# Performance work log

Measured on AMD Instinct MI355X. Metric: run time of the kernel, lower is better.

The kernel has to match this reference:

```python
import jax, jax.numpy as jnp
import numpy as np

N = 200000   # total nodes across batch
E = 800000   # total edges (avg degree 4)
G = 64       # number of graphs in batch
NGT = 30     # num gate types
EMB = 64     # gate_type_embed_dim
H = 128      # h_feats
INTER = 128  # inter_dim
EPS = 1e-12  # F.normalize eps


def _xavier(key, shape):
    fan_in, fan_out = shape
    std = np.sqrt(2.0 / (fan_in + fan_out))
    return jax.random.normal(key, shape, dtype=jnp.float32) * std


def setup_inputs() -> dict:
    key = jax.random.key(0)
    ks = jax.random.split(key, 12)
    gate_type = jax.random.randint(ks[0], (N,), 0, NGT)
    src = jax.random.randint(ks[1], (E,), 0, N)
    dst = jax.random.randint(ks[2], (E,), 0, N)
    w = jax.random.uniform(ks[3], (E, 3), dtype=jnp.float32)
    node2graph = (jnp.arange(N) * G) // N  # sorted segment ids, even split
    emb = jax.random.normal(ks[4], (NGT, EMB), dtype=jnp.float32)
    return {
        "gate_type": gate_type, "src": src, "dst": dst, "w": w,
        "node2graph": node2graph, "emb": emb,
        "W1_0": _xavier(ks[5], (EMB + 3, INTER)), "b1_0": jnp.zeros((INTER,), jnp.float32),
        "W2_0": _xavier(ks[6], (EMB + INTER, H)),
        "W1_1": _xavier(ks[7], (H + 3, INTER)), "b1_1": jnp.zeros((INTER,), jnp.float32),
        "W2_1": _xavier(ks[8], (H + INTER, H)),
        "W1_2": _xavier(ks[9], (H + 3, INTER)), "b1_2": jnp.zeros((INTER,), jnp.float32),
        "W2_2": _xavier(ks[10], (H + INTER, H)),
    }


def _qconv(h, src, dst, w, W1, b1, W2):
    # message: cat(h[src], w) per edge; linear1+ReLU per message; sum per dst node
    m = jnp.concatenate([h[src], w], axis=1)          # [E, in+3]
    t = jax.nn.relu(m @ W1 + b1)                      # [E, inter]
    h_N = jax.ops.segment_sum(t, dst, num_segments=h.shape[0])  # [N, inter]
    h_lin = jax.nn.relu(jnp.concatenate([h, h_N], axis=1) @ W2)  # [N, out]
    norm = jnp.linalg.norm(h_lin, axis=-1, keepdims=True)
    return h_lin / jnp.maximum(norm, EPS)             # F.normalize(p=2, dim=-1)


def reference(gate_type, src, dst, w, node2graph, emb,
              W1_0, b1_0, W2_0, W1_1, b1_1, W2_1, W1_2, b1_2, W2_2):
    h = emb[gate_type]                                # [N, EMB]
    layers = [(W1_0, b1_0, W2_0), (W1_1, b1_1, W2_1), (W1_2, b1_2, W2_2)]
    readouts = []
    for W1, b1, W2 in layers:
        h = _qconv(h, src, dst, w, W1, b1, W2)
        readouts.append(jax.ops.segment_sum(h, node2graph, num_segments=G))  # [G, H]
    return h, jnp.concatenate(readouts, axis=1)       # [N,H], [G, 3H]
```

## Files before the change

kernel.cpp:

```cpp
#include <hip/hip_runtime.h>
#include <hip/hip_bf16.h>
#include <hip/hip_fp16.h>

typedef _Float16 half8 __attribute__((ext_vector_type(8)));
typedef _Float16 half4 __attribute__((ext_vector_type(4)));
typedef _Float16 h2    __attribute__((ext_vector_type(2)));
typedef float floatx4 __attribute__((ext_vector_type(4)));

__device__ __forceinline__ _Float16 f2h(float f) { return (_Float16)f; }


__global__ void fill_dummy_kernel(int4* __restrict__ eData, int cap, int N, int NGT)
{
    int i = blockIdx.x * 256 + threadIdx.x;
    if (i < cap) { int4 v = {N | (NGT << 24), N, 0, 0}; eData[i] = v; }
}

__global__ void hist_kernel(const int* __restrict__ dst, int* __restrict__ cnt, int E)
{
    int e = blockIdx.x * 256 + threadIdx.x;
    if (e < E) atomicAdd(&cnt[dst[e]], 1);
}

__global__ void scan1p_kernel(const int* __restrict__ cnt, int* __restrict__ offP,
                              int n, int* __restrict__ blockSums)
{
    __shared__ int sm[256];
    const int t = threadIdx.x;
    const int base = blockIdx.x * 1024 + t * 4;
    int v[4]; int s = 0;
#pragma unroll
    for (int i = 0; i < 4; ++i) {
        v[i] = (base + i < n) ? ((cnt[base + i] + 3) & ~3) : 0;
        s += v[i];
    }
    sm[t] = s; __syncthreads();
#pragma unroll
    for (int off = 1; off < 256; off <<= 1) {
        int y = (t >= off) ? sm[t - off] : 0;
        __syncthreads();
        if (t >= off) sm[t] += y;
        __syncthreads();
    }
    int excl = sm[t] - s;
    if (t == 255) blockSums[blockIdx.x] = sm[255];
    int run = excl;
#pragma unroll
    for (int i = 0; i < 4; ++i) {
        if (base + i < n) offP[base + i] = run;
        run += v[i];
    }
}

__global__ void scan2_kernel(int* __restrict__ blockSums, int nb)
{
    __shared__ int sm[256];
    const int t = threadIdx.x;
    int s = (t < nb) ? blockSums[t] : 0;
    sm[t] = s; __syncthreads();
#pragma unroll
    for (int off = 1; off < 256; off <<= 1) {
        int y = (t >= off) ? sm[t - off] : 0;
        __syncthreads();
        if (t >= off) sm[t] += y;
        __syncthreads();
    }
    if (t < nb) blockSums[t] = sm[t] - s;
}

__global__ void scan3_kernel(int* __restrict__ offP, int n, const int* __restrict__ blockSums)
{
    const int base = blockIdx.x * 1024 + threadIdx.x * 4;
    const int add = blockSums[blockIdx.x];
#pragma unroll
    for (int i = 0; i < 4; ++i)
        if (base + i < n) offP[base + i] += add;
}

__global__ void scatter_kernel(const int* __restrict__ src, const int* __restrict__ dst,
                               const float* __restrict__ w, const int* __restrict__ gt,
                               const int* __restrict__ offP, int* __restrict__ cur,
                               int4* __restrict__ eData, int E)
{
    int e = blockIdx.x * 256 + threadIdx.x;
    if (e >= E) return;
    int d = dst[e];
    int p = offP[d] + atomicAdd(&cur[d], 1);
    int s = src[e];
    h2 w01 = { f2h(w[(size_t)e * 3 + 0]), f2h(w[(size_t)e * 3 + 1]) };
    h2 w2o = { f2h(w[(size_t)e * 3 + 2]), (_Float16)1.0f };
    int4 v = { s | (gt[s] << 24), d,
               __builtin_bit_cast(int, w01), __builtin_bit_cast(int, w2o) };
    eData[p] = v;
}

__global__ void ginfo_kernel(const int4* __restrict__ eData,
                             const int* __restrict__ cnt, const int* __restrict__ offP,
                             unsigned* __restrict__ gInfo,
                             int nGroups, int N, int gpw)
{
    int g = blockIdx.x * 256 + threadIdx.x;
    if (g >= nGroups) return;
    const int* ei = (const int*)eData;
    int d = ei[16 * g + 1];
    if (d >= N) { gInfo[g] = 0xFFFFFFFFu; return; }
    int cntP = (cnt[d] + 3) & ~3;
    int gA = offP[d] >> 2;
    int gB = gA + (cntP >> 2) - 1;
    bool cross = (gA / gpw) != (gB / gpw);
    gInfo[g] = (unsigned)d | (cross ? 0x80000000u : 0u);
}

__global__ void wprep_kernel(const float* __restrict__ W, _Float16* __restrict__ out,
                             int K, int KP)
{
    int idx = blockIdx.x * 256 + threadIdx.x;
    if (idx >= 128 * KP) return;
    int f = idx / KP, k = idx % KP;
    float v = (k < K) ? W[(size_t)k * 128 + f] : 0.0f;
    out[idx] = f2h(v);
}

__global__ void wwprep_kernel(const float* __restrict__ W1, int rowOff,
                              _Float16* __restrict__ out)
{
    int idx = blockIdx.x * 256 + threadIdx.x;
    if (idx < 3 * 128) out[idx] = f2h(W1[(size_t)(rowOff + idx / 128) * 128 + (idx & 127)]);
}

__global__ void embW1_kernel(const float* __restrict__ emb, const float* __restrict__ W1,
                             const float* __restrict__ b1, _Float16* __restrict__ out, int NGT)
{
    int idx = blockIdx.x * 256 + threadIdx.x;
    if (idx >= (NGT + 1) * 128) return;
    int g = idx >> 7, f = idx & 127;
    float s = 0.0f;
    if (g < NGT) {
        s = b1[f];
        for (int k = 0; k < 64; ++k) s += emb[g * 64 + k] * W1[(size_t)k * 128 + f];
    }
    out[idx] = f2h(s);
}

__global__ void embW2_kernel(const float* __restrict__ emb, const float* __restrict__ W2,
                             float* __restrict__ out, int NGT)
{
    int idx = blockIdx.x * 256 + threadIdx.x;
    if (idx >= NGT * 128) return;
    int g = idx >> 7, f = idx & 127;
    float s = 0.0f;
    for (int k = 0; k < 64; ++k) s += emb[g * 64 + k] * W2[(size_t)k * 128 + f];
    out[idx] = s;
}

__global__ void __launch_bounds__(512, 2)
hw1_kernel(const _Float16* __restrict__ hA,
           const _Float16* __restrict__ WT,
           const float* __restrict__ b1,
           _Float16* __restrict__ out,
           int N, int tilesPerWave, int nTiles)
{
    __shared__ __align__(16) _Float16 lds[128 * 128];
    const int tid = threadIdx.x;
    for (int s = tid; s < 128 * 16; s += 512) {
        const int row = s / 16, seg = s % 16;
        half8 v = *(const half8*)(WT + (size_t)row * 128 + seg * 8);
        *(half8*)(&lds[row * 128 + ((seg ^ (row & 7)) * 8)]) = v;
    }
    __syncthreads();

    const int lane = tid & 63;
    const int wv   = tid >> 6;
    const int lRow = lane & 15;
    const int lGrp = lane >> 4;

    float b1v[8];
#pragma unroll
    for (int jt = 0; jt < 8; ++jt) b1v[jt] = b1[jt * 16 + lRow];

    const int wave = blockIdx.x * 8 + wv;
    const int t0 = wave * tilesPerWave;
    const int t1 = min(t0 + tilesPerWave, nTiles);

    for (int tile = t0; tile < t1; ++tile) {
        const int i0 = tile * 16;
        const int iA = min(i0 + lRow, N - 1);
        half8 a[4];
#pragma unroll
        for (int kc = 0; kc < 4; ++kc)
            a[kc] = *(const half8*)(hA + (size_t)iA * 128 + kc * 32 + lGrp * 8);

        floatx4 acc[8] = {};
#pragma unroll
        for (int jt = 0; jt < 8; ++jt) {
            const int row = jt * 16 + lRow;
            const int sw = row & 7;
#pragma unroll
            for (int kc = 0; kc < 4; ++kc) {
                half8 b = *(const half8*)(&lds[row * 128 + (((kc * 4 + lGrp) ^ sw) * 8)]);
                acc[jt] = __builtin_amdgcn_mfma_f32_16x16x32_f16(a[kc], b, acc[jt], 0, 0, 0);
            }
        }
#pragma unroll
        for (int r = 0; r < 4; ++r) {
            const int i = i0 + lGrp * 4 + r;
            if (i < N) {
#pragma unroll
                for (int jt = 0; jt < 8; ++jt)
                    out[(size_t)i * 128 + jt * 16 + lRow] = f2h(acc[jt][r] + b1v[jt]);
            }
        }
    }
}

template<bool L0, bool H16>
__global__ void __launch_bounds__(256, 4)
edgeW_kernel(const _Float16* __restrict__ T,
             const _Float16* __restrict__ Wwh,
             const int4* __restrict__ eData,
             const unsigned* __restrict__ gInfo,
             void* __restrict__ hNv, int groupsPerWave, int nGroups)
{
    const int tid  = threadIdx.x;
    const int lane = tid & 63;
    const int wv   = tid >> 6;
    const int eidx = lane >> 4;
    const int c8   = (lane & 15) * 8;

    const h2 z = {(_Float16)0.0f, (_Float16)0.0f};
    h2 w0[4], w1[4], w2[4];
#pragma unroll
    for (int j = 0; j < 4; ++j) {
        w0[j] = *(const h2*)(Wwh + 0 * 128 + c8 + 2 * j);
        w1[j] = *(const h2*)(Wwh + 1 * 128 + c8 + 2 * j);
        w2[j] = *(const h2*)(Wwh + 2 * 128 + c8 + 2 * j);
    }

    const int wave = blockIdx.x * 4 + wv;
    const int g0 = wave * groupsPerWave;
    const int g1 = min(g0 + groupsPerWave, nGroups);
    if (g0 >= g1) return;

    int runD = -1; bool runCross = false;
    h2 a0 = z, a1 = z, a2 = z, a3 = z;

    auto flush = [&]() {
        if (runD < 0) return;
        h2 s0 = a0, s1 = a1, s2 = a2, s3 = a3;
#pragma unroll
        for (int m = 16; m <= 32; m <<= 1) {
            int t0_ = __shfl_xor(__builtin_bit_cast(int, s0), m);
            int t1_ = __shfl_xor(__builtin_bit_cast(int, s1), m);
            int t2_ = __shfl_xor(__builtin_bit_cast(int, s2), m);
            int t3_ = __shfl_xor(__builtin_bit_cast(int, s3), m);
            s0 = s0 + __builtin_bit_cast(h2, t0_);
            s1 = s1 + __builtin_bit_cast(h2, t1_);
            s2 = s2 + __builtin_bit_cast(h2, t2_);
            s3 = s3 + __builtin_bit_cast(h2, t3_);
        }
        if (lane < 16) {
            if (H16) {
                if (runCross) {
                    __half2* p = (__half2*)((__half*)hNv + (size_t)runD * 128 + c8);
                    unsafeAtomicAdd(p + 0, __builtin_bit_cast(__half2, s0));
                    unsafeAtomicAdd(p + 1, __builtin_bit_cast(__half2, s1));
                    unsafeAtomicAdd(p + 2, __builtin_bit_cast(__half2, s2));
                    unsafeAtomicAdd(p + 3, __builtin_bit_cast(__half2, s3));
                } else {
                    int4 pk = { __builtin_bit_cast(int, s0), __builtin_bit_cast(int, s1),
                                __builtin_bit_cast(int, s2), __builtin_bit_cast(int, s3) };
                    *(int4*)((__half*)hNv + (size_t)runD * 128 + c8) = pk;
                }
            } else {
                float f[8] = {(float)s0[0], (float)s0[1], (float)s1[0], (float)s1[1],
                              (float)s2[0], (float)s2[1], (float)s3[0], (float)s3[1]};
                float* p = (float*)hNv + (size_t)runD * 128 + c8;
                if (runCross) {
#pragma unroll
                    for (int j = 0; j < 8; ++j) unsafeAtomicAdd(p + j, f[j]);
                } else {
                    floatx4 q0 = {f[0], f[1], f[2], f[3]};
                    floatx4 q1 = {f[4], f[5], f[6], f[7]};
                    *(floatx4*)(p) = q0;
                    *(floatx4*)(p + 4) = q1;
                }
            }
        }
    };

    for (int g = g0; g < g1; ++g) {
        const unsigned gi = gInfo[g];
        if (gi == 0xFFFFFFFFu) break;
        const int dG = (int)(gi & 0xFFFFFFu);

        const int4 e = eData[g * 4 + eidx];
        const int r_ = L0 ? (e.x >> 24) : (e.x & 0xFFFFFF);
        const half8 Tv = *(const half8*)(T + (size_t)r_ * 128 + c8);
        const h2 w01 = __builtin_bit_cast(h2, e.z);
        const h2 w2o = __builtin_bit_cast(h2, e.w);

        h2 m0 = h2{Tv[0], Tv[1]} + w01[0] * w0[0] + w01[1] * w1[0] + w2o[0] * w2[0];
        h2 m1 = h2{Tv[2], Tv[3]} + w01[0] * w0[1] + w01[1] * w1[1] + w2o[0] * w2[1];
        h2 m2 = h2{Tv[4], Tv[5]} + w01[0] * w0[2] + w01[1] * w1[2] + w2o[0] * w2[2];
        h2 m3 = h2{Tv[6], Tv[7]} + w01[0] * w0[3] + w01[1] * w1[3] + w2o[0] * w2[3];
        h2 r0 = __builtin_elementwise_max(m0, z);
        h2 r1 = __builtin_elementwise_max(m1, z);
        h2 r2 = __builtin_elementwise_max(m2, z);
        h2 r3 = __builtin_elementwise_max(m3, z);

        if (dG == runD) {
            a0 = a0 + r0; a1 = a1 + r1; a2 = a2 + r2; a3 = a3 + r3;
        } else {
            flush();
            runD = dG; runCross = (gi >> 31) != 0;
            a0 = r0; a1 = r1; a2 = r2; a3 = r3;
        }
    }
    flush();
}

template<bool H16, bool L0, bool LAST>
__global__ void __launch_bounds__(512, 2)
node_kernel(const _Float16* __restrict__ hA,
            const void* __restrict__ hNv,
            const _Float16* __restrict__ W2T,
            const float* __restrict__ embW2,
            const int* __restrict__ gt,
            const int* __restrict__ n2g,
            _Float16* __restrict__ hOut,
            float* __restrict__ fOut,
            float* __restrict__ readout,
            int N, int tilesPerWave, int nTiles, int layerOff)
{
    constexpr int K2  = L0 ? 128 : 256;
    constexpr int KCA = L0 ? 0 : 4;
    constexpr int KC  = K2 / 32;
    constexpr int SPR = K2 / 8;
    __shared__ __align__(16) _Float16 lds[128 * K2];

    const int tid = threadIdx.x;
    for (int s = tid; s < 128 * SPR; s += 512) {
        const int row = s / SPR, seg = s % SPR;
        half8 v = *(const half8*)(W2T + (size_t)row * K2 + seg * 8);
        *(half8*)(&lds[row * K2 + ((seg ^ (row & 7)) * 8)]) = v;
    }
    __syncthreads();

    const int lane = tid & 63;
    const int wv   = tid >> 6;
    const int lRow = lane & 15;
    const int lGrp = lane >> 4;
    const int wave = blockIdx.x * 8 + wv;
    const int t0 = wave * tilesPerWave;
    const int t1 = min(t0 + tilesPerWave, nTiles);
    if (t0 >= t1) return;

    int gCur = -1; float racc[8];
#pragma unroll
    for (int jt = 0; jt < 8; ++jt) racc[jt] = 0.0f;

    auto loadA = [&](int i0, half8 (&afrag)[KC]) {
        const int iA = min(i0 + lRow, N - 1);
#pragma unroll
        for (int kc = 0; kc < KCA; ++kc)
            afrag[kc] = *(const half8*)(hA + (size_t)iA * 128 + kc * 32 + lGrp * 8);
        if (H16) {
            const _Float16* hN = (const _Float16*)hNv;
#pragma unroll
            for (int kc = KCA; kc < KC; ++kc)
                afrag[kc] = *(const half8*)(hN + (size_t)iA * 128 + (kc - KCA) * 32 + lGrp * 8);
        } else {
            const float* hN = (const float*)hNv;
#pragma unroll
            for (int kc = KCA; kc < KC; ++kc) {
                const float* p = hN + (size_t)iA * 128 + (kc - KCA) * 32 + lGrp * 8;
                floatx4 f0 = *(const floatx4*)(p);
                floatx4 f1 = *(const floatx4*)(p + 4);
                half8 a;
#pragma unroll
                for (int i = 0; i < 4; ++i) { a[i] = f2h(f0[i]); a[i + 4] = f2h(f1[i]); }
                afrag[kc] = a;
            }
        }
    };

    auto epilogue = [&](int i0, floatx4 (&acc)[8]) {
        if (L0) {
#pragma unroll
            for (int r = 0; r < 4; ++r) {
                const int i = min(i0 + lGrp * 4 + r, N - 1);
                const int g_t = gt[i];
#pragma unroll
                for (int jt = 0; jt < 8; ++jt)
                    acc[jt][r] += embW2[(size_t)g_t * 128 + jt * 16 + lRow];
            }
        }
        float scl[4];
#pragma unroll
        for (int r = 0; r < 4; ++r) {
            float s = 0.f;
#pragma unroll
            for (int jt = 0; jt < 8; ++jt) {
                float v = fmaxf(acc[jt][r], 0.0f);
                s += v * v;
            }
#pragma unroll
            for (int m = 1; m <= 8; m <<= 1) s += __shfl_xor(s, m);
            scl[r] = 1.0f / fmaxf(sqrtf(s), 1e-12f);
        }
#pragma unroll
        for (int r = 0; r < 4; ++r) {
            const int i = i0 + lGrp * 4 + r;
            if (i < N) {
#pragma unroll
                for (int jt = 0; jt < 8; ++jt) {
                    float v = fmaxf(acc[jt][r], 0.0f) * scl[r];
                    if (LAST) fOut[(size_t)i * 128 + jt * 16 + lRow] = v;
                    else      hOut[(size_t)i * 128 + jt * 16 + lRow] = f2h(v);
                }
            }
        }
        const int gFirst = n2g[min(i0, N - 1)];
        const int gLast  = n2g[min(i0 + 15, N - 1)];
        if (gFirst == gLast && i0 + 15 < N) {
            if (gFirst != gCur) {
                if (gCur >= 0 && lane < 16) {
#pragma unroll
                    for (int jt = 0; jt < 8; ++jt)
                        unsafeAtomicAdd(&readout[(size_t)gCur * 384 + layerOff + jt * 16 + lane], racc[jt]);
                }
                gCur = gFirst;
#pragma unroll
                for (int jt = 0; jt < 8; ++jt) racc[jt] = 0.0f;
            }
#pragma unroll
            for (int jt = 0; jt < 8; ++jt) {
                float t = 0.f;
#pragma unroll
                for (int r = 0; r < 4; ++r) t += fmaxf(acc[jt][r], 0.0f) * scl[r];
                t += __shfl_xor(t, 16);
                t += __shfl_xor(t, 32);
                racc[jt] += t;
            }
        } else {
            if (gCur >= 0 && lane < 16) {
#pragma unroll
                for (int jt = 0; jt < 8; ++jt)
                    unsafeAtomicAdd(&readout[(size_t)gCur * 384 + layerOff + jt * 16 + lane], racc[jt]);
            }
            gCur = -1;
#pragma unroll
            for (int jt = 0; jt < 8; ++jt) racc[jt] = 0.0f;
#pragma unroll
            for (int r = 0; r < 4; ++r) {
                const int i = i0 + lGrp * 4 + r;
                if (i < N) {
                    const int g = n2g[i];
#pragma unroll
                    for (int jt = 0; jt < 8; ++jt) {
                        float v = fmaxf(acc[jt][r], 0.0f) * scl[r];
                        unsafeAtomicAdd(&readout[(size_t)g * 384 + layerOff + jt * 16 + lRow], v);
                    }
                }
            }
        }
    };

    for (int tile = t0; tile < t1; tile += 2) {
        const bool has2 = (tile + 1 < t1);
        const int i0a = tile * 16;
        const int i0b = has2 ? (tile + 1) * 16 : i0a;

        half8 afA[KC], afB[KC];
        loadA(i0a, afA);
        loadA(i0b, afB);

        floatx4 accA[8] = {}, accB[8] = {};
#pragma unroll
        for (int jt = 0; jt < 8; ++jt) {
            const int rb = (jt * 16 + lRow) * K2;
            const int sw = (jt * 16 + lRow) & 7;
#pragma unroll
            for (int kc = 0; kc < KC; ++kc) {
                half8 b = *(const half8*)(&lds[rb + (((kc * 4 + lGrp) ^ sw) * 8)]);
                accA[jt] = __builtin_amdgcn_mfma_f32_16x16x32_f16(afA[kc], b, accA[jt], 0, 0, 0);
                accB[jt] = __builtin_amdgcn_mfma_f32_16x16x32_f16(afB[kc], b, accB[jt], 0, 0, 0);
            }
        }
        epilogue(i0a, accA);
        if (has2) epilogue(i0b, accB);
    }
    if (gCur >= 0 && lane < 16) {
#pragma unroll
        for (int jt = 0; jt < 8; ++jt)
            unsafeAtomicAdd(&readout[(size_t)gCur * 384 + layerOff + jt * 16 + lane], racc[jt]);
    }
}

extern "C" void kernel_launch(void* const* d_in, const int* in_sizes, int n_in,
                              void* d_out, int out_size, void* d_ws, size_t ws_size,
                              hipStream_t stream)
{
    const int*   gate_type = (const int*)d_in[0];
    const int*   src  = (const int*)d_in[1];
    const int*   dst  = (const int*)d_in[2];
    const float* wE   = (const float*)d_in[3];
    const int*   n2g  = (const int*)d_in[4];
    const float* emb  = (const float*)d_in[5];
    const float* W1_0 = (const float*)d_in[6];
    const float* b1_0 = (const float*)d_in[7];
    const float* W2_0 = (const float*)d_in[8];
    const float* W1_1 = (const float*)d_in[9];
    const float* b1_1 = (const float*)d_in[10];
    const float* W2_1 = (const float*)d_in[11];
    const float* W1_2 = (const float*)d_in[12];
    const float* b1_2 = (const float*)d_in[13];
    const float* W2_2 = (const float*)d_in[14];

    const int N = in_sizes[0];
    const int E = in_sizes[1];
    const int NGT = in_sizes[5] / 64;
    const int cap = (E + 3 * N + 15) & ~15;

    char* ws = (char*)d_ws;
    size_t off = 0;
    auto alloc = [&](size_t bytes) { void* p = ws + off; off = (off + bytes + 255) & ~255ULL; return p; };
    _Float16* hBuf  = (_Float16*)alloc((size_t)N * 128 * 2);
    int4*     eData = (int4*)alloc(((size_t)cap + 16) * 16);
    unsigned* gInfo = (unsigned*)alloc(((size_t)cap / 4 + 4) * 4);
    int*      cnt   = (int*)alloc((size_t)N * 4);
    int*      offP  = (int*)alloc((size_t)N * 4);
    int*      cur   = (int*)alloc((size_t)N * 4);
    int*      bSums = (int*)alloc(256 * 4);
    _Float16* W1T1  = (_Float16*)alloc((size_t)128 * 128 * 2);
    _Float16* W1T2  = (_Float16*)alloc((size_t)128 * 128 * 2);
    _Float16* W2T0  = (_Float16*)alloc((size_t)128 * 128 * 2);
    _Float16* W2T1  = (_Float16*)alloc((size_t)128 * 256 * 2);
    _Float16* W2T2  = (_Float16*)alloc((size_t)128 * 256 * 2);
    _Float16* Wwh0  = (_Float16*)alloc((size_t)3 * 128 * 2);
    _Float16* Wwh1  = (_Float16*)alloc((size_t)3 * 128 * 2);
    _Float16* Wwh2  = (_Float16*)alloc((size_t)3 * 128 * 2);
    _Float16* eW1b  = (_Float16*)alloc((size_t)(NGT + 1) * 128 * 2);
    float*    eW2   = (float*)alloc((size_t)NGT * 128 * 4);
    _Float16* hW1b  = (_Float16*)alloc(((size_t)N + 1) * 128 * 2);
    size_t hn16_off = off;
    const bool h16 = (ws_size >= hn16_off + (size_t)N * 128 * 2 + 256);
    _Float16* hN16 = (_Float16*)alloc((size_t)N * 128 * 2);

    float* readout = (float*)d_out + (size_t)N * 128;
    void*  hN      = h16 ? (void*)hN16 : (void*)d_out;

    const int nGroups = cap / 4;
    const int nTiles  = (N + 15) / 16;
    const int EB = 2048;
    const int gpw = (nGroups + EB * 4 - 1) / (EB * 4);
    const int NB = 256;
    const int tpwN = (nTiles + NB * 8 - 1) / (NB * 8);
    const int HB = 256;
    const int tpwH = (nTiles + HB * 8 - 1) / (HB * 8);
    const int nb = (N + 1023) / 1024;

    hipMemsetAsync(cnt, 0, (size_t)N * 4, stream);
    hipMemsetAsync(cur, 0, (size_t)N * 4, stream);
    hipMemsetAsync(hW1b + (size_t)N * 128, 0, 256, stream);
    fill_dummy_kernel<<<(cap + 16 + 255) / 256, 256, 0, stream>>>(eData, cap + 16, N, NGT);
    hist_kernel<<<(E + 255) / 256, 256, 0, stream>>>(dst, cnt, E);
    scan1p_kernel<<<nb, 256, 0, stream>>>(cnt, offP, N, bSums);
    scan2_kernel<<<1, 256, 0, stream>>>(bSums, nb);
    scan3_kernel<<<nb, 256, 0, stream>>>(offP, N, bSums);
    scatter_kernel<<<(E + 255) / 256, 256, 0, stream>>>(src, dst, wE, gate_type,
                                                        offP, cur, eData, E);
    ginfo_kernel<<<(nGroups + 255) / 256, 256, 0, stream>>>(eData, cnt, offP, gInfo,
                                                            nGroups, N, gpw);

    embW1_kernel<<<((NGT + 1) * 128 + 255) / 256, 256, 0, stream>>>(emb, W1_0, b1_0, eW1b, NGT);
    embW2_kernel<<<(NGT * 128 + 255) / 256, 256, 0, stream>>>(emb, W2_0, eW2, NGT);
    wprep_kernel<<<(128 * 128 + 255) / 256, 256, 0, stream>>>(W1_1, W1T1, 128, 128);
    wprep_kernel<<<(128 * 128 + 255) / 256, 256, 0, stream>>>(W1_2, W1T2, 128, 128);
    wprep_kernel<<<(128 * 128 + 255) / 256, 256, 0, stream>>>(W2_0 + (size_t)64 * 128, W2T0, 128, 128);
    wprep_kernel<<<(128 * 256 + 255) / 256, 256, 0, stream>>>(W2_1, W2T1, 256, 256);
    wprep_kernel<<<(128 * 256 + 255) / 256, 256, 0, stream>>>(W2_2, W2T2, 256, 256);
    wwprep_kernel<<<2, 256, 0, stream>>>(W1_0, 64, Wwh0);
    wwprep_kernel<<<2, 256, 0, stream>>>(W1_1, 128, Wwh1);
    wwprep_kernel<<<2, 256, 0, stream>>>(W1_2, 128, Wwh2);

    if (h16) {
        hipMemsetAsync(readout, 0, (size_t)(out_size - N * 128) * 4, stream);
        hipMemsetAsync(hN16, 0, (size_t)N * 128 * 2, stream);
        edgeW_kernel<true, true><<<EB, 256, 0, stream>>>(eW1b, Wwh0, eData, gInfo, hN, gpw, nGroups);
        node_kernel<true, true, false><<<NB, 512, 0, stream>>>(nullptr, hN, W2T0, eW2, gate_type, n2g,
                                                               hBuf, nullptr, readout, N, tpwN, nTiles, 0);
        hw1_kernel<<<HB, 512, 0, stream>>>(hBuf, W1T1, b1_1, hW1b, N, tpwH, nTiles);
        hipMemsetAsync(hN16, 0, (size_t)N * 128 * 2, stream);
        edgeW_kernel<false, true><<<EB, 256, 0, stream>>>(hW1b, Wwh1, eData, gInfo, hN, gpw, nGroups);
        node_kernel<true, false, false><<<NB, 512, 0, stream>>>(hBuf, hN, W2T1, nullptr, nullptr, n2g,
                                                                hBuf, nullptr, readout, N, tpwN, nTiles, 128);
        hw1_kernel<<<HB, 512, 0, stream>>>(hBuf, W1T2, b1_2, hW1b, N, tpwH, nTiles);
        hipMemsetAsync(hN16, 0, (size_t)N * 128 * 2, stream);
        edgeW_kernel<false, true><<<EB, 256, 0, stream>>>(hW1b, Wwh2, eData, gInfo, hN, gpw, nGroups);
        node_kernel<true, false, true><<<NB, 512, 0, stream>>>(hBuf, hN, W2T2, nullptr, nullptr, n2g,
                                                               nullptr, (float*)d_out, readout, N, tpwN, nTiles, 256);
    } else {
        hipMemsetAsync(d_out, 0, (size_t)out_size * 4, stream);
        edgeW_kernel<true, false><<<EB, 256, 0, stream>>>(eW1b, Wwh0, eData, gInfo, hN, gpw, nGroups);
        node_kernel<false, true, false><<<NB, 512, 0, stream>>>(nullptr, hN, W2T0, eW2, gate_type, n2g,
                                                                hBuf, nullptr, readout, N, tpwN, nTiles, 0);
        hw1_kernel<<<HB, 512, 0, stream>>>(hBuf, W1T1, b1_1, hW1b, N, tpwH, nTiles);
        hipMemsetAsync(d_out, 0, (size_t)N * 128 * 4, stream);
        edgeW_kernel<false, false><<<EB, 256, 0, stream>>>(hW1b, Wwh1, eData, gInfo, hN, gpw, nGroups);
        node_kernel<false, false, false><<<NB, 512, 0, stream>>>(hBuf, hN, W2T1, nullptr, nullptr, n2g,
                                                                 hBuf, nullptr, readout, N, tpwN, nTiles, 128);
        hw1_kernel<<<HB, 512, 0, stream>>>(hBuf, W1T2, b1_2, hW1b, N, tpwH, nTiles);
        hipMemsetAsync(d_out, 0, (size_t)N * 128 * 4, stream);
        edgeW_kernel<false, false><<<EB, 256, 0, stream>>>(hW1b, Wwh2, eData, gInfo, hN, gpw, nGroups);
        node_kernel<false, false, true><<<NB, 512, 0, stream>>>(hBuf, hN, W2T2, nullptr, nullptr, n2g,
                                                                nullptr, (float*)d_out, readout, N, tpwN, nTiles, 256);
    }
}
```

Baseline: 504.5 us.

## Zero only boundary and isolated hN rows; record edge ranks in histogram pass

```diff
diff --git a/kernel.cpp b/kernel.cpp
--- a/kernel.cpp
+++ b/kernel.cpp
@@ -16,10 +16,11 @@
     if (i < cap) { int4 v = {N | (NGT << 24), N, 0, 0}; eData[i] = v; }
 }
 
-__global__ void hist_kernel(const int* __restrict__ dst, int* __restrict__ cnt, int E)
+__global__ void histrank_kernel(const int* __restrict__ dst, int* __restrict__ cnt,
+                                int* __restrict__ rank, int E)
 {
     int e = blockIdx.x * 256 + threadIdx.x;
-    if (e < E) atomicAdd(&cnt[dst[e]], 1);
+    if (e < E) rank[e] = atomicAdd(&cnt[dst[e]], 1);
 }
 
 __global__ void scan1p_kernel(const int* __restrict__ cnt, int* __restrict__ offP,
@@ -79,13 +80,13 @@
 
 __global__ void scatter_kernel(const int* __restrict__ src, const int* __restrict__ dst,
                                const float* __restrict__ w, const int* __restrict__ gt,
-                               const int* __restrict__ offP, int* __restrict__ cur,
+                               const int* __restrict__ offP, const int* __restrict__ rank,
                                int4* __restrict__ eData, int E)
 {
     int e = blockIdx.x * 256 + threadIdx.x;
     if (e >= E) return;
     int d = dst[e];
-    int p = offP[d] + atomicAdd(&cur[d], 1);
+    int p = offP[d] + rank[e];
     int s = src[e];
     h2 w01 = { f2h(w[(size_t)e * 3 + 0]), f2h(w[(size_t)e * 3 + 1]) };
     h2 w2o = { f2h(w[(size_t)e * 3 + 2]), (_Float16)1.0f };
@@ -111,46 +112,87 @@
     gInfo[g] = (unsigned)d | (cross ? 0x80000000u : 0u);
 }
 
-__global__ void wprep_kernel(const float* __restrict__ W, _Float16* __restrict__ out,
-                             int K, int KP)
+__global__ void nodelists_kernel(const int* __restrict__ cnt, const int* __restrict__ offP,
+                                 int N, int gpw,
+                                 int* __restrict__ zCnt, int* __restrict__ zList,
+                                 int* __restrict__ cCnt, int* __restrict__ cList)
+{
+    int d = blockIdx.x * 256 + threadIdx.x;
+    if (d >= N) return;
+    int c = cnt[d];
+    if (c == 0) { zList[atomicAdd(zCnt, 1)] = d; return; }
+    int cntP = (c + 3) & ~3;
+    int gA = offP[d] >> 2;
+    int gB = gA + (cntP >> 2) - 1;
+    if (gA / gpw != gB / gpw) cList[atomicAdd(cCnt, 1)] = d;
+}
+
+__global__ void zero_rows_kernel(const int* __restrict__ list, const int* __restrict__ cntPtr,
+                                 _Float16* __restrict__ hN)
+{
+    const int n = *cntPtr * 16;
+    for (int i = blockIdx.x * 256 + threadIdx.x; i < n; i += gridDim.x * 256) {
+        const int row = list[i >> 4], c = (i & 15) * 8;
+        int4 zz = {0, 0, 0, 0};
+        *(int4*)(hN + (size_t)row * 128 + c) = zz;
+    }
+}
+
+__global__ void prep_all_kernel(const float* __restrict__ emb,
+                                const float* __restrict__ W1_0, const float* __restrict__ b1_0,
+                                const float* __restrict__ b1_1, const float* __restrict__ b1_2,
+                                const float* __restrict__ W1_1, const float* __restrict__ W1_2,
+                                const float* __restrict__ W2_0, const float* __restrict__ W2_1,
+                                const float* __restrict__ W2_2,
+                                _Float16* __restrict__ eW1b, float* __restrict__ eW2,
+                                _Float16* __restrict__ W1T1, _Float16* __restrict__ W1T2,
+                                _Float16* __restrict__ W2T0, _Float16* __restrict__ W2T1,
+                                _Float16* __restrict__ W2T2,
+                                _Float16* __restrict__ Wwh0, _Float16* __restrict__ Wwh1,
+                                _Float16* __restrict__ Wwh2, int NGT)
 {
     int idx = blockIdx.x * 256 + threadIdx.x;
-    if (idx >= 128 * KP) return;
-    int f = idx / KP, k = idx % KP;
-    float v = (k < K) ? W[(size_t)k * 128 + f] : 0.0f;
-    out[idx] = f2h(v);
-}
-
-__global__ void wwprep_kernel(const float* __restrict__ W1, int rowOff,
-                              _Float16* __restrict__ out)
-{
-    int idx = blockIdx.x * 256 + threadIdx.x;
-    if (idx < 3 * 128) out[idx] = f2h(W1[(size_t)(rowOff + idx / 128) * 128 + (idx & 127)]);
-}
-
-__global__ void embW1_kernel(const float* __restrict__ emb, const float* __restrict__ W1,
-                             const float* __restrict__ b1, _Float16* __restrict__ out, int NGT)
-{
-    int idx = blockIdx.x * 256 + threadIdx.x;
-    if (idx >= (NGT + 1) * 128) return;
-    int g = idx >> 7, f = idx & 127;
-    float s = 0.0f;
-    if (g < NGT) {
-        s = b1[f];
-        for (int k = 0; k < 64; ++k) s += emb[g * 64 + k] * W1[(size_t)k * 128 + f];
-    }
-    out[idx] = f2h(s);
-}
-
-__global__ void embW2_kernel(const float* __restrict__ emb, const float* __restrict__ W2,
-                             float* __restrict__ out, int NGT)
-{
-    int idx = blockIdx.x * 256 + threadIdx.x;
-    if (idx >= NGT * 128) return;
-    int g = idx >> 7, f = idx & 127;
-    float s = 0.0f;
-    for (int k = 0; k < 64; ++k) s += emb[g * 64 + k] * W2[(size_t)k * 128 + f];
-    out[idx] = s;
+    const int nE1 = (NGT + 1) * 128;
+    if (idx < nE1) {
+        int g = idx >> 7, f = idx & 127;
+        float s = 0.0f;
+        if (g < NGT) {
+            s = b1_0[f];
+            for (int k = 0; k < 64; ++k) s += emb[g * 64 + k] * W1_0[(size_t)k * 128 + f];
+        }
+        eW1b[idx] = f2h(s);
+        return;
+    }
+    idx -= nE1;
+    const int nE2 = NGT * 128;
+    if (idx < nE2) {
+        int g = idx >> 7, f = idx & 127;
+        float s = 0.0f;
+        for (int k = 0; k < 64; ++k) s += emb[g * 64 + k] * W2_0[(size_t)k * 128 + f];
+        eW2[idx] = s;
+        return;
+    }
+    idx -= nE2;
+    if (idx < 16384) { int f = idx >> 7, k = idx & 127;
+        W1T1[idx] = f2h(W1_1[(size_t)k * 128 + f]); return; }
+    idx -= 16384;
+    if (idx < 16384) { int f = idx >> 7, k = idx & 127;
+        W1T2[idx] = f2h(W1_2[(size_t)k * 128 + f]); return; }
+    idx -= 16384;
+    if (idx < 16384) { int f = idx >> 7, k = idx & 127;
+        W2T0[idx] = f2h(W2_0[(size_t)(64 + k) * 128 + f]); return; }
+    idx -= 16384;
+    if (idx < 32768) { int f = idx >> 8, k = idx & 255;
+        W2T1[idx] = f2h(W2_1[(size_t)k * 128 + f]); return; }
+    idx -= 32768;
+    if (idx < 32768) { int f = idx >> 8, k = idx & 255;
+        W2T2[idx] = f2h(W2_2[(size_t)k * 128 + f]); return; }
+    idx -= 32768;
+    if (idx < 384) { Wwh0[idx] = f2h(W1_0[(size_t)(64 + idx / 128) * 128 + (idx & 127)]); return; }
+    idx -= 384;
+    if (idx < 384) { Wwh1[idx] = f2h(W1_1[(size_t)(128 + idx / 128) * 128 + (idx & 127)]); return; }
+    idx -= 384;
+    if (idx < 384) { Wwh2[idx] = f2h(W1_2[(size_t)(128 + idx / 128) * 128 + (idx & 127)]); return; }
 }
 
 __global__ void __launch_bounds__(512, 2)
@@ -530,8 +572,11 @@
     unsigned* gInfo = (unsigned*)alloc(((size_t)cap / 4 + 4) * 4);
     int*      cnt   = (int*)alloc((size_t)N * 4);
     int*      offP  = (int*)alloc((size_t)N * 4);
-    int*      cur   = (int*)alloc((size_t)N * 4);
+    int*      rank  = (int*)alloc((size_t)E * 4);
     int*      bSums = (int*)alloc(256 * 4);
+    int*      zCnts = (int*)alloc(256);
+    int*      zList = (int*)alloc((size_t)N * 4);
+    int*      cList = (int*)alloc((size_t)N * 4);
     _Float16* W1T1  = (_Float16*)alloc((size_t)128 * 128 * 2);
     _Float16* W1T2  = (_Float16*)alloc((size_t)128 * 128 * 2);
     _Float16* W2T0  = (_Float16*)alloc((size_t)128 * 128 * 2);
@@ -559,44 +604,42 @@
     const int HB = 256;
     const int tpwH = (nTiles + HB * 8 - 1) / (HB * 8);
     const int nb = (N + 1023) / 1024;
+    const int prepTot = (NGT + 1) * 128 + NGT * 128 + 3 * 16384 + 2 * 32768 + 3 * 384;
 
     hipMemsetAsync(cnt, 0, (size_t)N * 4, stream);
-    hipMemsetAsync(cur, 0, (size_t)N * 4, stream);
+    hipMemsetAsync(zCnts, 0, 8, stream);
     hipMemsetAsync(hW1b + (size_t)N * 128, 0, 256, stream);
     fill_dummy_kernel<<<(cap + 16 + 255) / 256, 256, 0, stream>>>(eData, cap + 16, N, NGT);
-    hist_kernel<<<(E + 255) / 256, 256, 0, stream>>>(dst, cnt, E);
+    histrank_kernel<<<(E + 255) / 256, 256, 0, stream>>>(dst, cnt, rank, E);
     scan1p_kernel<<<nb, 256, 0, stream>>>(cnt, offP, N, bSums);
     scan2_kernel<<<1, 256, 0, stream>>>(bSums, nb);
     scan3_kernel<<<nb, 256, 0, stream>>>(offP, N, bSums);
     scatter_kernel<<<(E + 255) / 256, 256, 0, stream>>>(src, dst, wE, gate_type,
-                                                        offP, cur, eData, E);
+                                                        offP, rank, eData, E);
     ginfo_kernel<<<(nGroups + 255) / 256, 256, 0, stream>>>(eData, cnt, offP, gInfo,
                                                             nGroups, N, gpw);
-
-    embW1_kernel<<<((NGT + 1) * 128 + 255) / 256, 256, 0, stream>>>(emb, W1_0, b1_0, eW1b, NGT);
-    embW2_kernel<<<(NGT * 128 + 255) / 256, 256, 0, stream>>>(emb, W2_0, eW2, NGT);
-    wprep_kernel<<<(128 * 128 + 255) / 256, 256, 0, stream>>>(W1_1, W1T1, 128, 128);
-    wprep_kernel<<<(128 * 128 + 255) / 256, 256, 0, stream>>>(W1_2, W1T2, 128, 128);
-    wprep_kernel<<<(128 * 128 + 255) / 256, 256, 0, stream>>>(W2_0 + (size_t)64 * 128, W2T0, 128, 128);
-    wprep_kernel<<<(128 * 256 + 255) / 256, 256, 0, stream>>>(W2_1, W2T1, 256, 256);
-    wprep_kernel<<<(128 * 256 + 255) / 256, 256, 0, stream>>>(W2_2, W2T2, 256, 256);
-    wwprep_kernel<<<2, 256, 0, stream>>>(W1_0, 64, Wwh0);
-    wwprep_kernel<<<2, 256, 0, stream>>>(W1_1, 128, Wwh1);
-    wwprep_kernel<<<2, 256, 0, stream>>>(W1_2, 128, Wwh2);
+    nodelists_kernel<<<(N + 255) / 256, 256, 0, stream>>>(cnt, offP, N, gpw,
+                                                          zCnts, zList, zCnts + 1, cList);
+    prep_all_kernel<<<(prepTot + 255) / 256, 256, 0, stream>>>(emb, W1_0, b1_0, b1_1, b1_2,
+                                                               W1_1, W1_2, W2_0, W2_1, W2_2,
+                                                               eW1b, eW2, W1T1, W1T2,
+                                                               W2T0, W2T1, W2T2,
+                                                               Wwh0, Wwh1, Wwh2, NGT);
 
     if (h16) {
         hipMemsetAsync(readout, 0, (size_t)(out_size - N * 128) * 4, stream);
-        hipMemsetAsync(hN16, 0, (size_t)N * 128 * 2, stream);
+        zero_rows_kernel<<<64, 256, 0, stream>>>(zList, zCnts, hN16);
+        zero_rows_kernel<<<64, 256, 0, stream>>>(cList, zCnts + 1, hN16);
         edgeW_kernel<true, true><<<EB, 256, 0, stream>>>(eW1b, Wwh0, eData, gInfo, hN, gpw, nGroups);
         node_kernel<true, true, false><<<NB, 512, 0, stream>>>(nullptr, hN, W2T0, eW2, gate_type, n2g,
                                                                hBuf, nullptr, readout, N, tpwN, nTiles, 0);
         hw1_kernel<<<HB, 512, 0, stream>>>(hBuf, W1T1, b1_1, hW1b, N, tpwH, nTiles);
-        hipMemsetAsync(hN16, 0, (size_t)N * 128 * 2, stream);
+        zero_rows_kernel<<<64, 256, 0, stream>>>(cList, zCnts + 1, hN16);
         edgeW_kernel<false, true><<<EB, 256, 0, stream>>>(hW1b, Wwh1, eData, gInfo, hN, gpw, nGroups);
         node_kernel<true, false, false><<<NB, 512, 0, stream>>>(hBuf, hN, W2T1, nullptr, nullptr, n2g,
                                                                 hBuf, nullptr, readout, N, tpwN, nTiles, 128);
         hw1_kernel<<<HB, 512, 0, stream>>>(hBuf, W1T2, b1_2, hW1b, N, tpwH, nTiles);
-        hipMemsetAsync(hN16, 0, (size_t)N * 128 * 2, stream);
+        zero_rows_kernel<<<64, 256, 0, stream>>>(cList, zCnts + 1, hN16);
         edgeW_kernel<false, true><<<EB, 256, 0, stream>>>(hW1b, Wwh2, eData, gInfo, hN, gpw, nGroups);
         node_kernel<true, false, true><<<NB, 512, 0, stream>>>(hBuf, hN, W2T2, nullptr, nullptr, n2g,
                                                                nullptr, (float*)d_out, readout, N, tpwN, nTiles, 256);
```

Result: no change. 498.7 us (-1.2%).
